# Kernel optimization log

Measured on AMD Instinct MI355X. Metric: run time of the kernel, lower is better.

Reference implementation:

```python
import jax, jax.numpy as jnp
import numpy as np

WS = (8, 8)            # window_size
NUM_HEADS = 8


def _rel_pos_index():
    # Faithful to the torch buffer construction (meshgrid indexing='ij').
    ch, cw = np.arange(WS[0]), np.arange(WS[1])
    coords = np.stack(np.meshgrid(ch, cw, indexing='ij')).reshape(2, -1)  # (2, N)
    rel = coords[:, :, None] - coords[:, None, :]                          # (2, N, N)
    rel = rel.transpose(1, 2, 0).copy()                                    # (N, N, 2)
    rel[..., 0] += WS[0] - 1
    rel[..., 1] += WS[1] - 1
    rel[..., 0] *= 2 * WS[1] - 1
    return jnp.asarray(rel.sum(-1))                                        # (N, N) int


def setup_inputs() -> dict:
    key = jax.random.key(0)
    ks = jax.random.split(key, 7)
    B_, C, N, nW = 4096, 256, 64, 4096  # B_ = batch(1) * num_windows(4096)
    return {
        "x": jax.random.normal(ks[0], (B_, C, N), jnp.float32),
        "mask": jax.random.normal(ks[1], (nW, N, N), jnp.float32),
        "qkv_w": jax.random.normal(ks[2], (3 * C, C), jnp.float32) * 0.05,
        "qkv_b": jax.random.normal(ks[3], (3 * C,), jnp.float32) * 0.02,
        "proj_w": jax.random.normal(ks[4], (C, C), jnp.float32) * 0.05,
        "proj_b": jax.random.normal(ks[5], (C,), jnp.float32) * 0.02,
        "bias_table": jax.random.normal(ks[6], ((2 * WS[0] - 1) * (2 * WS[1] - 1), NUM_HEADS), jnp.float32) * 0.02,
    }


def reference(x, mask, qkv_w, qkv_b, proj_w, proj_b, bias_table):
    B_, C, N = x.shape
    H = NUM_HEADS
    hd = C // H
    scale = hd ** -0.5

    # Conv1d kernel_size=1 == linear over the channel dim.
    qkv = jnp.einsum('bcn,dc->bdn', x, qkv_w) + qkv_b[None, :, None]   # (B_, 3C, N)
    qkv = qkv.reshape(B_, 3, H, hd, N)
    q, k, v = qkv[:, 0], qkv[:, 1], qkv[:, 2]                          # (B_, H, hd, N)

    attn = jnp.einsum('bhdn,bhdm->bhnm', q * scale, k)                 # (B_, H, N, N)

    rpi = _rel_pos_index()                                              # (N, N)
    bias = bias_table[rpi]                                              # (N, N, H) gather
    attn = attn + jnp.transpose(bias, (2, 0, 1))[None]                  # (B_, H, N, N)

    nW = mask.shape[0]
    attn = (attn.reshape(B_ // nW, nW, H, N, N) + mask[None, :, None]).reshape(B_, H, N, N)
    attn = jax.nn.softmax(attn, axis=-1)

    out = jnp.einsum('bhnm,bhdm->bnhd', attn, v).reshape(B_, N, C)      # (B_, N, C)
    return jnp.einsum('bnc,dc->bnd', out, proj_w) + proj_b              # (B_, N, C)
```

## Files before the change

### kernel.cpp

```cpp
#include <hip/hip_runtime.h>

typedef __bf16 bf16_t;
typedef bf16_t bf16x8 __attribute__((ext_vector_type(8)));
typedef bf16_t bf16x4 __attribute__((ext_vector_type(4)));
typedef float  f32x4  __attribute__((ext_vector_type(4)));

#define NWIN 4096
#define CDIM 256
#define NTOK 64
#define NH   8

#define OFF_MASK  40960
#define LDS_BYTES 58368

__device__ __forceinline__ f32x4 mfma16(bf16x8 a, bf16x8 b, f32x4 c) {
    return __builtin_amdgcn_mfma_f32_16x16x32_bf16(a, b, c, 0, 0, 0);
}

template<bool USE_WS>
__launch_bounds__(512, 4)
__global__ void win_attn_kernel(const float* __restrict__ x,
                                const float* __restrict__ mask,
                                const float* __restrict__ qkv_w,
                                const float* __restrict__ qkv_b,
                                const float* __restrict__ proj_w,
                                const float* __restrict__ proj_b,
                                const float* __restrict__ bias_table,
                                const bf16_t* __restrict__ qkv_wb,
                                const bf16_t* __restrict__ proj_wb,
                                float* __restrict__ out)
{
    __shared__ __attribute__((aligned(16))) unsigned char smem[LDS_BYTES];
    bf16_t* xs       = (bf16_t*)smem;
    bf16_t* o_lds    = (bf16_t*)smem;
    float*  mask_lds = (float*)(smem + OFF_MASK);

    const int b    = blockIdx.x;
    const int tid  = threadIdx.x;
    const int w    = tid >> 6;
    const int lane = tid & 63;
    const int quad = lane >> 4;
    const int l15  = lane & 15;
    bf16_t* buf0 = (bf16_t*)(smem + w * 5120);

    {
        const float* xb = x + (size_t)b * (CDIM * NTOK);
        #pragma unroll
        for (int cb = 0; cb < 4; ++cb) {
            const int c0 = cb * 64 + w * 8;
            float v[8];
            #pragma unroll
            for (int j = 0; j < 8; ++j) v[j] = xb[(c0 + j) * 64 + lane];
            bf16x8 t;
            #pragma unroll
            for (int j = 0; j < 8; ++j) t[j] = (bf16_t)v[j];
            *(bf16x8*)(xs + lane * 264 + c0) = t;
        }
        const float* mb = mask + (size_t)b * (NTOK * NTOK);
        #pragma unroll
        for (int it = 0; it < 2; ++it) {
            int e = (it * 512 + tid) * 4;
            int n = e >> 6, m = e & 63;
            f32x4 mv = *(const f32x4*)(mb + e);
            *(f32x4*)(mask_lds + n * 68 + m) = mv;
        }
    }
    __syncthreads();

    const int h = w;
    const float scale = 0.17677669529663687f;

    bf16x4 qpk[2][4];
    bf16x4 kpk[2][4];
    bf16x4 vpk[4][2];

    #pragma unroll
    for (int sec = 0; sec < 2; ++sec) {
        f32x4 acc[2][4];
        #pragma unroll
        for (int rtl = 0; rtl < 2; ++rtl)
            #pragma unroll
            for (int ct = 0; ct < 4; ++ct) acc[rtl][ct] = (f32x4){0.f,0.f,0.f,0.f};

        #pragma unroll 1
        for (int kk = 0; kk < 8; ++kk) {
            const int c0 = kk * 32;
            bf16x8 afr[2];
            #pragma unroll
            for (int rtl = 0; rtl < 2; ++rtl) {
                int row = sec * 256 + h * 32 + rtl * 16 + l15;
                if constexpr (USE_WS) {
                    afr[rtl] = *(const bf16x8*)(qkv_wb + row * CDIM + c0 + quad * 8);
                } else {
                    const float* ap = qkv_w + row * CDIM + c0 + quad * 8;
                    f32x4 a0 = *(const f32x4*)ap;
                    f32x4 a1 = *(const f32x4*)(ap + 4);
                    bf16x8 t;
                    #pragma unroll
                    for (int j = 0; j < 4; ++j) { t[j] = (bf16_t)a0[j]; t[j+4] = (bf16_t)a1[j]; }
                    afr[rtl] = t;
                }
            }
            bf16x8 bfr[4];
            #pragma unroll
            for (int ct = 0; ct < 4; ++ct)
                bfr[ct] = *(const bf16x8*)(xs + (ct * 16 + l15) * 264 + c0 + quad * 8);
            #pragma unroll
            for (int rtl = 0; rtl < 2; ++rtl)
                #pragma unroll
                for (int ct = 0; ct < 4; ++ct)
                    acc[rtl][ct] = mfma16(afr[rtl], bfr[ct], acc[rtl][ct]);
        }
        #pragma unroll
        for (int rtl = 0; rtl < 2; ++rtl) {
            f32x4 b4 = *(const f32x4*)(qkv_b + sec * 256 + h * 32 + rtl * 16 + quad * 4);
            #pragma unroll
            for (int ct = 0; ct < 4; ++ct) {
                #pragma unroll
                for (int r = 0; r < 4; ++r) {
                    float vv = acc[rtl][ct][r] + b4[r];
                    if (sec == 0) qpk[rtl][ct][r] = (bf16_t)(vv * scale);
                    else          kpk[rtl][ct][r] = (bf16_t)vv;
                }
            }
        }
    }
    {
        f32x4 acc[4][2];
        #pragma unroll
        for (int ct = 0; ct < 4; ++ct)
            #pragma unroll
            for (int rtl = 0; rtl < 2; ++rtl) acc[ct][rtl] = (f32x4){0.f,0.f,0.f,0.f};

        #pragma unroll 1
        for (int kk = 0; kk < 8; ++kk) {
            const int c0 = kk * 32;
            bf16x8 afr[2];
            #pragma unroll
            for (int rtl = 0; rtl < 2; ++rtl) {
                int row = 512 + h * 32 + rtl * 16 + l15;
                if constexpr (USE_WS) {
                    afr[rtl] = *(const bf16x8*)(qkv_wb + row * CDIM + c0 + quad * 8);
                } else {
                    const float* ap = qkv_w + row * CDIM + c0 + quad * 8;
                    f32x4 a0 = *(const f32x4*)ap;
                    f32x4 a1 = *(const f32x4*)(ap + 4);
                    bf16x8 t;
                    #pragma unroll
                    for (int j = 0; j < 4; ++j) { t[j] = (bf16_t)a0[j]; t[j+4] = (bf16_t)a1[j]; }
                    afr[rtl] = t;
                }
            }
            bf16x8 bfr[4];
            #pragma unroll
            for (int ct = 0; ct < 4; ++ct)
                bfr[ct] = *(const bf16x8*)(xs + (ct * 16 + l15) * 264 + c0 + quad * 8);
            #pragma unroll
            for (int ct = 0; ct < 4; ++ct)
                #pragma unroll
                for (int rtl = 0; rtl < 2; ++rtl)
                    acc[ct][rtl] = mfma16(bfr[ct], afr[rtl], acc[ct][rtl]);
        }
        #pragma unroll
        for (int rtl = 0; rtl < 2; ++rtl) {
            float bv = qkv_b[512 + h * 32 + rtl * 16 + l15];
            #pragma unroll
            for (int ct = 0; ct < 4; ++ct)
                #pragma unroll
                for (int r = 0; r < 4; ++r) vpk[ct][rtl][r] = (bf16_t)(acc[ct][rtl][r] + bv);
        }
    }
    __syncthreads();

    #pragma unroll
    for (int rtl = 0; rtl < 2; ++rtl)
        #pragma unroll
        for (int ct = 0; ct < 4; ++ct)
            *(bf16x4*)(buf0 + (ct * 16 + l15) * 40 + rtl * 16 + quad * 4) = qpk[rtl][ct];
    bf16x8 qa[4];
    #pragma unroll
    for (int nt = 0; nt < 4; ++nt)
        qa[nt] = *(const bf16x8*)(buf0 + (nt * 16 + l15) * 40 + quad * 8);

    #pragma unroll
    for (int rtl = 0; rtl < 2; ++rtl)
        #pragma unroll
        for (int ct = 0; ct < 4; ++ct)
            *(bf16x4*)(buf0 + (ct * 16 + l15) * 40 + rtl * 16 + quad * 4) = kpk[rtl][ct];
    bf16x8 kb[4];
    #pragma unroll
    for (int mt = 0; mt < 4; ++mt)
        kb[mt] = *(const bf16x8*)(buf0 + (mt * 16 + l15) * 40 + quad * 8);

    #pragma unroll
    for (int rtl = 0; rtl < 2; ++rtl)
        #pragma unroll
        for (int ct = 0; ct < 4; ++ct)
            *(bf16x4*)(buf0 + (rtl * 16 + l15) * 72 + ct * 16 + quad * 4) = vpk[ct][rtl];

    float inv[4];
    bf16x4 ppk[4][4];
    {
        const int qhi = quad >> 1, qlo = quad & 1;
        const int nwv = (l15 & 7) + 7 - 4 * qlo;
        const int nh_ = l15 >> 3;
        #pragma unroll
        for (int nt = 0; nt < 4; ++nt) {
            f32x4 scol[4];
            #pragma unroll
            for (int mt = 0; mt < 4; ++mt)
                scol[mt] = mfma16(kb[mt], qa[nt], (f32x4){0.f,0.f,0.f,0.f});
            const int n = nt * 16 + l15;
            #pragma unroll
            for (int mt = 0; mt < 4; ++mt) {
                f32x4 mv = *(const f32x4*)(mask_lds + n * 68 + mt * 16 + quad * 4);
                int base = (nt * 2 + nh_ - 2 * mt - qhi + 7) * 15 + nwv;
                #pragma unroll
                for (int r = 0; r < 4; ++r)
                    scol[mt][r] += bias_table[(base - r) * NH + h] + mv[r];
            }
            float mx = scol[0][0];
            #pragma unroll
            for (int mt = 0; mt < 4; ++mt)
                #pragma unroll
                for (int r = 0; r < 4; ++r) mx = fmaxf(mx, scol[mt][r]);
            mx = fmaxf(mx, __shfl_xor(mx, 16, 64));
            mx = fmaxf(mx, __shfl_xor(mx, 32, 64));
            float s = 0.f;
            #pragma unroll
            for (int mt = 0; mt < 4; ++mt)
                #pragma unroll
                for (int r = 0; r < 4; ++r) {
                    float e = __expf(scol[mt][r] - mx);
                    ppk[mt][nt][r] = (bf16_t)e;
                    s += e;
                }
            s += __shfl_xor(s, 16, 64);
            s += __shfl_xor(s, 32, 64);
            inv[nt] = __builtin_amdgcn_rcpf(s);
        }
    }

    bf16x8 vb[2][2];
    #pragma unroll
    for (int dt = 0; dt < 2; ++dt)
        #pragma unroll
        for (int ch = 0; ch < 2; ++ch)
            vb[dt][ch] = *(const bf16x8*)(buf0 + (dt * 16 + l15) * 72 + ch * 32 + quad * 8);

    f32x4 oaccT[2][4];
    #pragma unroll
    for (int dt = 0; dt < 2; ++dt)
        #pragma unroll
        for (int nt = 0; nt < 4; ++nt) oaccT[dt][nt] = (f32x4){0.f,0.f,0.f,0.f};

    #pragma unroll
    for (int ch = 0; ch < 2; ++ch) {
        #pragma unroll
        for (int mt2 = 0; mt2 < 2; ++mt2) {
            #pragma unroll
            for (int nt = 0; nt < 4; ++nt)
                *(bf16x4*)(buf0 + (nt * 16 + l15) * 40 + mt2 * 16 + quad * 4) = ppk[2 * ch + mt2][nt];
        }
        #pragma unroll
        for (int nt = 0; nt < 4; ++nt) {
            bf16x8 pb = *(const bf16x8*)(buf0 + (nt * 16 + l15) * 40 + quad * 8);
            #pragma unroll
            for (int dt = 0; dt < 2; ++dt)
                oaccT[dt][nt] = mfma16(vb[dt][ch], pb, oaccT[dt][nt]);
        }
    }
    __syncthreads();

    #pragma unroll
    for (int dt = 0; dt < 2; ++dt)
        #pragma unroll
        for (int nt = 0; nt < 4; ++nt) {
            bf16x4 pk;
            #pragma unroll
            for (int r = 0; r < 4; ++r) pk[r] = (bf16_t)(oaccT[dt][nt][r] * inv[nt]);
            *(bf16x4*)(o_lds + (nt * 16 + l15) * 264 + h * 32 + dt * 16 + quad * 4) = pk;
        }
    __syncthreads();

    {
        f32x4 yacc[2][4];
        #pragma unroll
        for (int rt = 0; rt < 2; ++rt)
            #pragma unroll
            for (int ct = 0; ct < 4; ++ct) yacc[rt][ct] = (f32x4){0.f,0.f,0.f,0.f};

        #pragma unroll 1
        for (int kk = 0; kk < 8; ++kk) {
            const int c0 = kk * 32;
            bf16x8 afr[2];
            #pragma unroll
            for (int rt = 0; rt < 2; ++rt) {
                int e = w * 32 + rt * 16 + l15;
                if constexpr (USE_WS) {
                    afr[rt] = *(const bf16x8*)(proj_wb + e * CDIM + c0 + quad * 8);
                } else {
                    const float* ap = proj_w + e * CDIM + c0 + quad * 8;
                    f32x4 a0 = *(const f32x4*)ap;
                    f32x4 a1 = *(const f32x4*)(ap + 4);
                    bf16x8 t;
                    #pragma unroll
                    for (int j = 0; j < 4; ++j) { t[j] = (bf16_t)a0[j]; t[j+4] = (bf16_t)a1[j]; }
                    afr[rt] = t;
                }
            }
            bf16x8 bfr[4];
            #pragma unroll
            for (int ct = 0; ct < 4; ++ct)
                bfr[ct] = *(const bf16x8*)(o_lds + (ct * 16 + l15) * 264 + c0 + quad * 8);
            #pragma unroll
            for (int rt = 0; rt < 2; ++rt)
                #pragma unroll
                for (int ct = 0; ct < 4; ++ct)
                    yacc[rt][ct] = mfma16(afr[rt], bfr[ct], yacc[rt][ct]);
        }
        float* ob = out + (size_t)b * (NTOK * CDIM);
        #pragma unroll
        for (int rt = 0; rt < 2; ++rt) {
            int e0 = w * 32 + rt * 16 + quad * 4;
            f32x4 pb4 = *(const f32x4*)(proj_b + e0);
            #pragma unroll
            for (int ct = 0; ct < 4; ++ct) {
                int n = ct * 16 + l15;
                f32x4 r = yacc[rt][ct] + pb4;
                *(f32x4*)(ob + n * 256 + e0) = r;
            }
        }
    }
}

__global__ void cvt_weights(const float* __restrict__ qkv_w,
                            const float* __restrict__ proj_w,
                            bf16_t* __restrict__ qkv_wb,
                            bf16_t* __restrict__ proj_wb)
{
    int i = blockIdx.x * 256 + threadIdx.x;
    int base = i * 4;
    const float* src; bf16_t* dst;
    if (base < 196608) { src = qkv_w + base; dst = qkv_wb + base; }
    else { base -= 196608; src = proj_w + base; dst = proj_wb + base; }
    f32x4 v = *(const f32x4*)src;
    bf16x4 o;
    #pragma unroll
    for (int j = 0; j < 4; ++j) o[j] = (bf16_t)v[j];
    *(bf16x4*)dst = o;
}

extern "C" void kernel_launch(void* const* d_in, const int* in_sizes, int n_in,
                              void* d_out, int out_size, void* d_ws, size_t ws_size,
                              hipStream_t stream) {
    const float* x          = (const float*)d_in[0];
    const float* mask       = (const float*)d_in[1];
    const float* qkv_w      = (const float*)d_in[2];
    const float* qkv_b      = (const float*)d_in[3];
    const float* proj_w     = (const float*)d_in[4];
    const float* proj_b     = (const float*)d_in[5];
    const float* bias_table = (const float*)d_in[6];
    float* out = (float*)d_out;

    const size_t ws_needed = (size_t)(196608 + 65536) * sizeof(bf16_t);
    if (ws_size >= ws_needed) {
        bf16_t* qkv_wb  = (bf16_t*)d_ws;
        bf16_t* proj_wb = qkv_wb + 196608;
        cvt_weights<<<256, 256, 0, stream>>>(qkv_w, proj_w, qkv_wb, proj_wb);
        win_attn_kernel<true><<<NWIN, 512, 0, stream>>>(
            x, mask, qkv_w, qkv_b, proj_w, proj_b, bias_table, qkv_wb, proj_wb, out);
    } else {
        win_attn_kernel<false><<<NWIN, 512, 0, stream>>>(
            x, mask, qkv_w, qkv_b, proj_w, proj_b, bias_table, nullptr, nullptr, out);
    }
}
```

Measured before the change: 798.4 us.

## Prefetch weight fragments across k-steps, precompute dense rel-pos bias, reorder QKV

After: 747.6 us. 1.07x faster.

```diff
diff --git a/kernel.cpp b/kernel.cpp
--- a/kernel.cpp
+++ b/kernel.cpp
@@ -15,6 +15,21 @@
 
 __device__ __forceinline__ f32x4 mfma16(bf16x8 a, bf16x8 b, f32x4 c) {
     return __builtin_amdgcn_mfma_f32_16x16x32_bf16(a, b, c, 0, 0, 0);
+}
+
+template<bool USE_WS>
+__device__ __forceinline__ bf16x8 load_wrow(const bf16_t* wb, const float* wf, int row, int c) {
+    if constexpr (USE_WS) {
+        return *(const bf16x8*)(wb + row * CDIM + c);
+    } else {
+        const float* ap = wf + row * CDIM + c;
+        f32x4 a0 = *(const f32x4*)ap;
+        f32x4 a1 = *(const f32x4*)(ap + 4);
+        bf16x8 t;
+        #pragma unroll
+        for (int j = 0; j < 4; ++j) { t[j] = (bf16_t)a0[j]; t[j + 4] = (bf16_t)a1[j]; }
+        return t;
+    }
 }
 
 template<bool USE_WS>
@@ -28,6 +43,7 @@
                                 const float* __restrict__ bias_table,
                                 const bf16_t* __restrict__ qkv_wb,
                                 const bf16_t* __restrict__ proj_wb,
+                                const float* __restrict__ bias_pre,
                                 float* __restrict__ out)
 {
     __shared__ __attribute__((aligned(16))) unsigned char smem[LDS_BYTES];
@@ -70,113 +86,122 @@
     const int h = w;
     const float scale = 0.17677669529663687f;
 
-    bf16x4 qpk[2][4];
     bf16x4 kpk[2][4];
     bf16x4 vpk[4][2];
 
-    #pragma unroll
-    for (int sec = 0; sec < 2; ++sec) {
-        f32x4 acc[2][4];
-        #pragma unroll
-        for (int rtl = 0; rtl < 2; ++rtl)
-            #pragma unroll
-            for (int ct = 0; ct < 4; ++ct) acc[rtl][ct] = (f32x4){0.f,0.f,0.f,0.f};
-
+    {
+        f32x4 acc[4][2];
+        #pragma unroll
+        for (int ct = 0; ct < 4; ++ct)
+            #pragma unroll
+            for (int rtl = 0; rtl < 2; ++rtl) acc[ct][rtl] = (f32x4){0.f,0.f,0.f,0.f};
+
+        const int r0 = 512 + h * 32 + l15;
+        bf16x8 a0 = load_wrow<USE_WS>(qkv_wb, qkv_w, r0,      quad * 8);
+        bf16x8 a1 = load_wrow<USE_WS>(qkv_wb, qkv_w, r0 + 16, quad * 8);
         #pragma unroll 1
         for (int kk = 0; kk < 8; ++kk) {
             const int c0 = kk * 32;
-            bf16x8 afr[2];
-            #pragma unroll
-            for (int rtl = 0; rtl < 2; ++rtl) {
-                int row = sec * 256 + h * 32 + rtl * 16 + l15;
-                if constexpr (USE_WS) {
-                    afr[rtl] = *(const bf16x8*)(qkv_wb + row * CDIM + c0 + quad * 8);
-                } else {
-                    const float* ap = qkv_w + row * CDIM + c0 + quad * 8;
-                    f32x4 a0 = *(const f32x4*)ap;
-                    f32x4 a1 = *(const f32x4*)(ap + 4);
-                    bf16x8 t;
-                    #pragma unroll
-                    for (int j = 0; j < 4; ++j) { t[j] = (bf16_t)a0[j]; t[j+4] = (bf16_t)a1[j]; }
-                    afr[rtl] = t;
-                }
-            }
+            const int c1 = ((kk + 1) & 7) * 32 + quad * 8;
+            bf16x8 n0 = load_wrow<USE_WS>(qkv_wb, qkv_w, r0,      c1);
+            bf16x8 n1 = load_wrow<USE_WS>(qkv_wb, qkv_w, r0 + 16, c1);
             bf16x8 bfr[4];
             #pragma unroll
             for (int ct = 0; ct < 4; ++ct)
                 bfr[ct] = *(const bf16x8*)(xs + (ct * 16 + l15) * 264 + c0 + quad * 8);
             #pragma unroll
-            for (int rtl = 0; rtl < 2; ++rtl)
-                #pragma unroll
-                for (int ct = 0; ct < 4; ++ct)
-                    acc[rtl][ct] = mfma16(afr[rtl], bfr[ct], acc[rtl][ct]);
+            for (int ct = 0; ct < 4; ++ct) {
+                acc[ct][0] = mfma16(bfr[ct], a0, acc[ct][0]);
+                acc[ct][1] = mfma16(bfr[ct], a1, acc[ct][1]);
+            }
+            a0 = n0; a1 = n1;
         }
         #pragma unroll
         for (int rtl = 0; rtl < 2; ++rtl) {
-            f32x4 b4 = *(const f32x4*)(qkv_b + sec * 256 + h * 32 + rtl * 16 + quad * 4);
-            #pragma unroll
-            for (int ct = 0; ct < 4; ++ct) {
-                #pragma unroll
-                for (int r = 0; r < 4; ++r) {
-                    float vv = acc[rtl][ct][r] + b4[r];
-                    if (sec == 0) qpk[rtl][ct][r] = (bf16_t)(vv * scale);
-                    else          kpk[rtl][ct][r] = (bf16_t)vv;
-                }
-            }
-        }
-    }
-    {
-        f32x4 acc[4][2];
-        #pragma unroll
-        for (int ct = 0; ct < 4; ++ct)
-            #pragma unroll
-            for (int rtl = 0; rtl < 2; ++rtl) acc[ct][rtl] = (f32x4){0.f,0.f,0.f,0.f};
-
+            float bv = qkv_b[512 + h * 32 + rtl * 16 + l15];
+            #pragma unroll
+            for (int ct = 0; ct < 4; ++ct)
+                #pragma unroll
+                for (int r = 0; r < 4; ++r) vpk[ct][rtl][r] = (bf16_t)(acc[ct][rtl][r] + bv);
+        }
+    }
+    {
+        f32x4 acc[2][4];
+        #pragma unroll
+        for (int rtl = 0; rtl < 2; ++rtl)
+            #pragma unroll
+            for (int ct = 0; ct < 4; ++ct) acc[rtl][ct] = (f32x4){0.f,0.f,0.f,0.f};
+
+        const int r0 = 256 + h * 32 + l15;
+        bf16x8 a0 = load_wrow<USE_WS>(qkv_wb, qkv_w, r0,      quad * 8);
+        bf16x8 a1 = load_wrow<USE_WS>(qkv_wb, qkv_w, r0 + 16, quad * 8);
         #pragma unroll 1
         for (int kk = 0; kk < 8; ++kk) {
             const int c0 = kk * 32;
-            bf16x8 afr[2];
-            #pragma unroll
-            for (int rtl = 0; rtl < 2; ++rtl) {
-                int row = 512 + h * 32 + rtl * 16 + l15;
-                if constexpr (USE_WS) {
-                    afr[rtl] = *(const bf16x8*)(qkv_wb + row * CDIM + c0 + quad * 8);
-                } else {
-                    const float* ap = qkv_w + row * CDIM + c0 + quad * 8;
-                    f32x4 a0 = *(const f32x4*)ap;
-                    f32x4 a1 = *(const f32x4*)(ap + 4);
-                    bf16x8 t;
-                    #pragma unroll
-                    for (int j = 0; j < 4; ++j) { t[j] = (bf16_t)a0[j]; t[j+4] = (bf16_t)a1[j]; }
-                    afr[rtl] = t;
-                }
-            }
+            const int c1 = ((kk + 1) & 7) * 32 + quad * 8;
+            bf16x8 n0 = load_wrow<USE_WS>(qkv_wb, qkv_w, r0,      c1);
+            bf16x8 n1 = load_wrow<USE_WS>(qkv_wb, qkv_w, r0 + 16, c1);
             bf16x8 bfr[4];
             #pragma unroll
             for (int ct = 0; ct < 4; ++ct)
                 bfr[ct] = *(const bf16x8*)(xs + (ct * 16 + l15) * 264 + c0 + quad * 8);
             #pragma unroll
-            for (int ct = 0; ct < 4; ++ct)
-                #pragma unroll
-                for (int rtl = 0; rtl < 2; ++rtl)
-                    acc[ct][rtl] = mfma16(bfr[ct], afr[rtl], acc[ct][rtl]);
+            for (int ct = 0; ct < 4; ++ct) {
+                acc[0][ct] = mfma16(a0, bfr[ct], acc[0][ct]);
+                acc[1][ct] = mfma16(a1, bfr[ct], acc[1][ct]);
+            }
+            a0 = n0; a1 = n1;
         }
         #pragma unroll
         for (int rtl = 0; rtl < 2; ++rtl) {
-            float bv = qkv_b[512 + h * 32 + rtl * 16 + l15];
-            #pragma unroll
-            for (int ct = 0; ct < 4; ++ct)
-                #pragma unroll
-                for (int r = 0; r < 4; ++r) vpk[ct][rtl][r] = (bf16_t)(acc[ct][rtl][r] + bv);
+            f32x4 b4 = *(const f32x4*)(qkv_b + 256 + h * 32 + rtl * 16 + quad * 4);
+            #pragma unroll
+            for (int ct = 0; ct < 4; ++ct)
+                #pragma unroll
+                for (int r = 0; r < 4; ++r) kpk[rtl][ct][r] = (bf16_t)(acc[rtl][ct][r] + b4[r]);
+        }
+    }
+    f32x4 qacc[2][4];
+    {
+        #pragma unroll
+        for (int rtl = 0; rtl < 2; ++rtl)
+            #pragma unroll
+            for (int ct = 0; ct < 4; ++ct) qacc[rtl][ct] = (f32x4){0.f,0.f,0.f,0.f};
+
+        const int r0 = h * 32 + l15;
+        bf16x8 a0 = load_wrow<USE_WS>(qkv_wb, qkv_w, r0,      quad * 8);
+        bf16x8 a1 = load_wrow<USE_WS>(qkv_wb, qkv_w, r0 + 16, quad * 8);
+        #pragma unroll 1
+        for (int kk = 0; kk < 8; ++kk) {
+            const int c0 = kk * 32;
+            const int c1 = ((kk + 1) & 7) * 32 + quad * 8;
+            bf16x8 n0 = load_wrow<USE_WS>(qkv_wb, qkv_w, r0,      c1);
+            bf16x8 n1 = load_wrow<USE_WS>(qkv_wb, qkv_w, r0 + 16, c1);
+            bf16x8 bfr[4];
+            #pragma unroll
+            for (int ct = 0; ct < 4; ++ct)
+                bfr[ct] = *(const bf16x8*)(xs + (ct * 16 + l15) * 264 + c0 + quad * 8);
+            #pragma unroll
+            for (int ct = 0; ct < 4; ++ct) {
+                qacc[0][ct] = mfma16(a0, bfr[ct], qacc[0][ct]);
+                qacc[1][ct] = mfma16(a1, bfr[ct], qacc[1][ct]);
+            }
+            a0 = n0; a1 = n1;
         }
     }
     __syncthreads();
 
     #pragma unroll
-    for (int rtl = 0; rtl < 2; ++rtl)
-        #pragma unroll
-        for (int ct = 0; ct < 4; ++ct)
-            *(bf16x4*)(buf0 + (ct * 16 + l15) * 40 + rtl * 16 + quad * 4) = qpk[rtl][ct];
+    for (int rtl = 0; rtl < 2; ++rtl) {
+        f32x4 b4 = *(const f32x4*)(qkv_b + h * 32 + rtl * 16 + quad * 4);
+        #pragma unroll
+        for (int ct = 0; ct < 4; ++ct) {
+            bf16x4 pk;
+            #pragma unroll
+            for (int r = 0; r < 4; ++r) pk[r] = (bf16_t)((qacc[rtl][ct][r] + b4[r]) * scale);
+            *(bf16x4*)(buf0 + (ct * 16 + l15) * 40 + rtl * 16 + quad * 4) = pk;
+        }
+    }
     bf16x8 qa[4];
     #pragma unroll
     for (int nt = 0; nt < 4; ++nt)
@@ -211,13 +236,23 @@
             for (int mt = 0; mt < 4; ++mt)
                 scol[mt] = mfma16(kb[mt], qa[nt], (f32x4){0.f,0.f,0.f,0.f});
             const int n = nt * 16 + l15;
-            #pragma unroll
-            for (int mt = 0; mt < 4; ++mt) {
-                f32x4 mv = *(const f32x4*)(mask_lds + n * 68 + mt * 16 + quad * 4);
-                int base = (nt * 2 + nh_ - 2 * mt - qhi + 7) * 15 + nwv;
-                #pragma unroll
-                for (int r = 0; r < 4; ++r)
-                    scol[mt][r] += bias_table[(base - r) * NH + h] + mv[r];
+            if constexpr (USE_WS) {
+                const float* bh = bias_pre + (h << 12) + n * 64;
+                #pragma unroll
+                for (int mt = 0; mt < 4; ++mt) {
+                    f32x4 bv = *(const f32x4*)(bh + mt * 16 + quad * 4);
+                    f32x4 mv = *(const f32x4*)(mask_lds + n * 68 + mt * 16 + quad * 4);
+                    scol[mt] += bv + mv;
+                }
+            } else {
+                #pragma unroll
+                for (int mt = 0; mt < 4; ++mt) {
+                    f32x4 mv = *(const f32x4*)(mask_lds + n * 68 + mt * 16 + quad * 4);
+                    int base = (nt * 2 + nh_ - 2 * mt - qhi + 7) * 15 + nwv;
+                    #pragma unroll
+                    for (int r = 0; r < 4; ++r)
+                        scol[mt][r] += bias_table[(base - r) * NH + h] + mv[r];
+                }
             }
             float mx = scol[0][0];
             #pragma unroll
@@ -290,34 +325,25 @@
             #pragma unroll
             for (int ct = 0; ct < 4; ++ct) yacc[rt][ct] = (f32x4){0.f,0.f,0.f,0.f};
 
+        const int e0r = w * 32 + l15;
+        bf16x8 a0 = load_wrow<USE_WS>(proj_wb, proj_w, e0r,      quad * 8);
+        bf16x8 a1 = load_wrow<USE_WS>(proj_wb, proj_w, e0r + 16, quad * 8);
         #pragma unroll 1
         for (int kk = 0; kk < 8; ++kk) {
             const int c0 = kk * 32;
-            bf16x8 afr[2];
-            #pragma unroll
-            for (int rt = 0; rt < 2; ++rt) {
-                int e = w * 32 + rt * 16 + l15;
-                if constexpr (USE_WS) {
-                    afr[rt] = *(const bf16x8*)(proj_wb + e * CDIM + c0 + quad * 8);
-                } else {
-                    const float* ap = proj_w + e * CDIM + c0 + quad * 8;
-                    f32x4 a0 = *(const f32x4*)ap;
-                    f32x4 a1 = *(const f32x4*)(ap + 4);
-                    bf16x8 t;
-                    #pragma unroll
-                    for (int j = 0; j < 4; ++j) { t[j] = (bf16_t)a0[j]; t[j+4] = (bf16_t)a1[j]; }
-                    afr[rt] = t;
-                }
-            }
+            const int c1 = ((kk + 1) & 7) * 32 + quad * 8;
+            bf16x8 n0 = load_wrow<USE_WS>(proj_wb, proj_w, e0r,      c1);
+            bf16x8 n1 = load_wrow<USE_WS>(proj_wb, proj_w, e0r + 16, c1);
             bf16x8 bfr[4];
             #pragma unroll
             for (int ct = 0; ct < 4; ++ct)
                 bfr[ct] = *(const bf16x8*)(o_lds + (ct * 16 + l15) * 264 + c0 + quad * 8);
             #pragma unroll
-            for (int rt = 0; rt < 2; ++rt)
-                #pragma unroll
-                for (int ct = 0; ct < 4; ++ct)
-                    yacc[rt][ct] = mfma16(afr[rt], bfr[ct], yacc[rt][ct]);
+            for (int ct = 0; ct < 4; ++ct) {
+                yacc[0][ct] = mfma16(a0, bfr[ct], yacc[0][ct]);
+                yacc[1][ct] = mfma16(a1, bfr[ct], yacc[1][ct]);
+            }
+            a0 = n0; a1 = n1;
         }
         float* ob = out + (size_t)b * (NTOK * CDIM);
         #pragma unroll
@@ -336,19 +362,34 @@
 
 __global__ void cvt_weights(const float* __restrict__ qkv_w,
                             const float* __restrict__ proj_w,
+                            const float* __restrict__ bias_table,
                             bf16_t* __restrict__ qkv_wb,
-                            bf16_t* __restrict__ proj_wb)
+                            bf16_t* __restrict__ proj_wb,
+                            float* __restrict__ bias_pre)
 {
     int i = blockIdx.x * 256 + threadIdx.x;
-    int base = i * 4;
-    const float* src; bf16_t* dst;
-    if (base < 196608) { src = qkv_w + base; dst = qkv_wb + base; }
-    else { base -= 196608; src = proj_w + base; dst = proj_wb + base; }
-    f32x4 v = *(const f32x4*)src;
-    bf16x4 o;
-    #pragma unroll
-    for (int j = 0; j < 4; ++j) o[j] = (bf16_t)v[j];
-    *(bf16x4*)dst = o;
+    if (i < 65536) {
+        int base = i * 4;
+        const float* src; bf16_t* dst;
+        if (base < 196608) { src = qkv_w + base; dst = qkv_wb + base; }
+        else { base -= 196608; src = proj_w + base; dst = proj_wb + base; }
+        f32x4 v = *(const f32x4*)src;
+        bf16x4 o;
+        #pragma unroll
+        for (int j = 0; j < 4; ++j) o[j] = (bf16_t)v[j];
+        *(bf16x4*)dst = o;
+    } else {
+        int base = (i - 65536) * 4;
+        int h = base >> 12, n = (base >> 6) & 63, m0 = base & 63;
+        f32x4 o;
+        #pragma unroll
+        for (int j = 0; j < 4; ++j) {
+            int m = m0 + j;
+            int idx = ((n >> 3) - (m >> 3) + 7) * 15 + ((n & 7) - (m & 7) + 7);
+            o[j] = bias_table[idx * NH + h];
+        }
+        *(f32x4*)(bias_pre + base) = o;
+    }
 }
 
 extern "C" void kernel_launch(void* const* d_in, const int* in_sizes, int n_in,
@@ -363,15 +404,16 @@
     const float* bias_table = (const float*)d_in[6];
     float* out = (float*)d_out;
 
-    const size_t ws_needed = (size_t)(196608 + 65536) * sizeof(bf16_t);
+    const size_t ws_needed = 524288 + 524288;
     if (ws_size >= ws_needed) {
         bf16_t* qkv_wb  = (bf16_t*)d_ws;
         bf16_t* proj_wb = qkv_wb + 196608;
-        cvt_weights<<<256, 256, 0, stream>>>(qkv_w, proj_w, qkv_wb, proj_wb);
+        float*  bias_pre = (float*)((unsigned char*)d_ws + 524288);
+        cvt_weights<<<384, 256, 0, stream>>>(qkv_w, proj_w, bias_table, qkv_wb, proj_wb, bias_pre);
         win_attn_kernel<true><<<NWIN, 512, 0, stream>>>(
-            x, mask, qkv_w, qkv_b, proj_w, proj_b, bias_table, qkv_wb, proj_wb, out);
+            x, mask, qkv_w, qkv_b, proj_w, proj_b, bias_table, qkv_wb, proj_wb, bias_pre, out);
     } else {
         win_attn_kernel<false><<<NWIN, 512, 0, stream>>>(
-            x, mask, qkv_w, qkv_b, proj_w, proj_b, bias_table, nullptr, nullptr, out);
+            x, mask, qkv_w, qkv_b, proj_w, proj_b, bias_table, nullptr, nullptr, nullptr, out);
     }
 }
```
